# Kernel tuning notes

Measured on AMD Instinct MI355X. Metric: run time of the kernel, lower is better.

## Reference

```python
import jax, jax.numpy as jnp
import numpy as np

N, E = 50000, 800000
IN_DIM, HID, OUT, HEADS = 128, 128, 64, 4
C1 = HID // HEADS  # 32 per-head channels in gat1
NEG_SLOPE = 0.2


def _gat_conv(x, src, dst, W, a_src, a_dst, b, heads, ch):
    """PyG GATConv (inference): gather -> edge attention -> segment softmax -> scatter."""
    n = x.shape[0]
    h = (x @ W).reshape(n, heads, ch)                      # [N,H,C]
    alpha_src = jnp.einsum('nhc,hc->nh', h, a_src)         # [N,H]
    alpha_dst = jnp.einsum('nhc,hc->nh', h, a_dst)         # [N,H]
    e = jax.nn.leaky_relu(alpha_src[src] + alpha_dst[dst], NEG_SLOPE)  # [E,H]
    m = jax.ops.segment_max(e, dst, num_segments=n)        # per-target max (stable softmax)
    e = jnp.exp(e - m[dst])
    denom = jax.ops.segment_sum(e, dst, num_segments=n)
    alpha = e / (denom[dst] + 1e-16)                       # [E,H]
    out = jax.ops.segment_sum(h[src] * alpha[:, :, None], dst, num_segments=n)  # [N,H,C]
    return out.reshape(n, heads * ch) + b


def setup_inputs() -> dict:
    key = jax.random.key(0)
    ks = jax.random.split(key, 16)
    x = jax.random.normal(ks[0], (N, IN_DIM), dtype=jnp.float32)
    edge_index = jax.random.randint(ks[1], (2, E), 0, N, dtype=jnp.int64)
    s = lambda fan_in: 1.0 / np.sqrt(fan_in)
    return {
        'x': x,
        'edge_index': edge_index,
        'W1': jax.random.normal(ks[2], (IN_DIM, HEADS * C1), jnp.float32) * s(IN_DIM),
        'a_src1': jax.random.normal(ks[3], (HEADS, C1), jnp.float32) * s(C1),
        'a_dst1': jax.random.normal(ks[4], (HEADS, C1), jnp.float32) * s(C1),
        'b1': jnp.zeros((HID,), jnp.float32),
        'W2': jax.random.normal(ks[5], (HID, OUT), jnp.float32) * s(HID),
        'a_src2': jax.random.normal(ks[6], (1, OUT), jnp.float32) * s(OUT),
        'a_dst2': jax.random.normal(ks[7], (1, OUT), jnp.float32) * s(OUT),
        'b2': jnp.zeros((OUT,), jnp.float32),
        'pw1': jax.random.normal(ks[8], (OUT, OUT), jnp.float32) * s(OUT),
        'pb1': jnp.zeros((OUT,), jnp.float32),
        'pw2': jax.random.normal(ks[9], (OUT, OUT), jnp.float32) * s(OUT),
        'pb2': jnp.zeros((OUT,), jnp.float32),
    }


def reference(x, edge_index, W1, a_src1, a_dst1, b1, W2, a_src2, a_dst2, b2, pw1, pb1, pw2, pb2):
    n = x.shape[0]
    # PyG GATConv add_self_loops=True
    loops = jnp.arange(n, dtype=edge_index.dtype)
    src = jnp.concatenate([edge_index[0], loops])
    dst = jnp.concatenate([edge_index[1], loops])
    h = jax.nn.elu(_gat_conv(x, src, dst, W1, a_src1, a_dst1, b1, HEADS, C1))
    h = jax.nn.elu(_gat_conv(h, src, dst, W2, a_src2, a_dst2, b2, 1, OUT))
    # origin_proj: Linear -> ReLU -> Linear
    h = jax.nn.relu(h @ pw1 + pb1)
    return h @ pw2 + pb2
```

## Files before the change

### kernel.cpp

```cpp
#include <hip/hip_runtime.h>
#include <math.h>

#define N_NODES 50000
#define N_EDGES 800000
#define ET (N_EDGES + N_NODES)
#define IN_DIM 128
#define HID 128
#define OUT_DIM 64
#define BW 64
#define NBUCK ((N_NODES + BW - 1) / BW)
#define NBLK 256
#define EPB 3328

__device__ __forceinline__ float lrelu(float x){ return x >= 0.f ? x : 0.2f * x; }
__device__ __forceinline__ float eluf(float x){ return x > 0.f ? x : expm1f(x); }
__device__ __forceinline__ unsigned f2bf(float f){
    unsigned u = __float_as_uint(f);
    return (u + 0x7fffu + ((u >> 16) & 1u)) >> 16;
}
__device__ __forceinline__ float bflo(unsigned u){ return __uint_as_float(u << 16); }
__device__ __forceinline__ float bfhi(unsigned u){ return __uint_as_float(u & 0xffff0000u); }

__global__ __launch_bounds__(256) void k_count(const int* __restrict__ dst, int* __restrict__ C)
{
    __shared__ int cnt[NBUCK];
    const int tid = threadIdx.x, blk = blockIdx.x;
    for (int i = tid; i < NBUCK; i += 256) cnt[i] = 0;
    __syncthreads();
    #pragma unroll
    for (int j = 0; j < EPB / 256; j++) {
        const int e = blk * EPB + j * 256 + tid;
        if (e < ET) {
            const int d = (e < N_EDGES) ? dst[e] : (e - N_EDGES);
            atomicAdd(&cnt[d >> 6], 1);
        }
    }
    __syncthreads();
    for (int b = tid; b < NBUCK; b += 256) C[b * NBLK + blk] = cnt[b];
}

__global__ __launch_bounds__(256) void k_bsumA(const int* __restrict__ C, int* __restrict__ bsum2)
{
    __shared__ int red[4];
    int v = C[blockIdx.x * NBLK + threadIdx.x];
    #pragma unroll
    for (int off = 32; off > 0; off >>= 1) v += __shfl_down(v, off);
    if ((threadIdx.x & 63) == 0) red[threadIdx.x >> 6] = v;
    __syncthreads();
    if (threadIdx.x == 0) bsum2[blockIdx.x] = red[0] + red[1] + red[2] + red[3];
}

__global__ __launch_bounds__(1024) void k_bscanB(const int* __restrict__ bsum2, int* __restrict__ boff2)
{
    __shared__ int part[1024];
    const int t = threadIdx.x;
    int v = (t < NBUCK) ? bsum2[t] : 0;
    part[t] = v;
    __syncthreads();
    #pragma unroll
    for (int d = 1; d < 1024; d <<= 1) {
        int add = (t >= d) ? part[t - d] : 0;
        __syncthreads();
        part[t] += add;
        __syncthreads();
    }
    if (t < NBUCK) boff2[t] = part[t] - v;
    if (t == 0) boff2[NBUCK] = ET;
}

__global__ __launch_bounds__(256) void k_cscanC(const int* __restrict__ C,
                                                const int* __restrict__ boff2,
                                                int* __restrict__ Cs)
{
    __shared__ int part[256];
    const int t = threadIdx.x, b = blockIdx.x;
    int v = C[b * NBLK + t];
    part[t] = v;
    __syncthreads();
    #pragma unroll
    for (int d = 1; d < 256; d <<= 1) {
        int add = (t >= d) ? part[t - d] : 0;
        __syncthreads();
        part[t] += add;
        __syncthreads();
    }
    Cs[b * NBLK + t] = boff2[b] + part[t] - v;
}

__global__ __launch_bounds__(256) void k_part2(const int* __restrict__ src,
                                               const int* __restrict__ dst,
                                               const int* __restrict__ Cs,
                                               uint2* __restrict__ part)
{
    __shared__ int base[NBUCK];
    __shared__ int cnt[NBUCK];
    const int tid = threadIdx.x, blk = blockIdx.x;
    for (int b = tid; b < NBUCK; b += 256) { base[b] = Cs[b * NBLK + blk]; cnt[b] = 0; }
    __syncthreads();
    #pragma unroll
    for (int j = 0; j < EPB / 256; j++) {
        const int e = blk * EPB + j * 256 + tid;
        if (e < ET) {
            int s, d;
            if (e < N_EDGES) { s = src[e]; d = dst[e]; } else { s = d = e - N_EDGES; }
            const int b = d >> 6;
            const int r = atomicAdd(&cnt[b], 1);
            part[base[b] + r] = make_uint2((unsigned)d, (unsigned)s);
        }
    }
}

__global__ __launch_bounds__(256) void k_scat2(const int* __restrict__ boff2,
                                               const uint2* __restrict__ part,
                                               int* __restrict__ rowptr,
                                               int* __restrict__ csr_src)
{
    __shared__ int cnt64[BW];
    __shared__ int nbase[BW];
    const int b = blockIdx.x, tid = threadIdx.x;
    const int n0 = b * BW;
    const int lo = boff2[b], hi = boff2[b + 1];
    if (tid < BW) cnt64[tid] = 0;
    __syncthreads();
    for (int i = lo + tid; i < hi; i += 256) {
        atomicAdd(&cnt64[part[i].x & (BW - 1)], 1);
    }
    __syncthreads();
    if (tid < BW) {
        int v = cnt64[tid];
        int incl = v;
        #pragma unroll
        for (int off = 1; off < 64; off <<= 1) {
            int t2 = __shfl_up(incl, off);
            if (tid >= off) incl += t2;
        }
        const int excl = incl - v;
        nbase[tid] = excl;
        const int n = n0 + tid;
        if (n < N_NODES) rowptr[n] = lo + excl;
        cnt64[tid] = 0;
    }
    if (b == 0 && tid == 0) rowptr[N_NODES] = ET;
    __syncthreads();
    for (int i = lo + tid; i < hi; i += 256) {
        const uint2 p = part[i];
        const int dn = (int)p.x & (BW - 1);
        const int r = atomicAdd(&cnt64[dn], 1);
        csr_src[lo + nbase[dn] + r] = (int)p.y;
    }
}

__global__ __launch_bounds__(256, 3) void k_gemm1(
    const float* __restrict__ x, const float* __restrict__ W1,
    const float* __restrict__ a_s, const float* __restrict__ a_d,
    unsigned* __restrict__ h1b, float* __restrict__ as1, float* __restrict__ ad1)
{
    __shared__ float sW[32 * 128];
    __shared__ float sx[128 * 32];
    float4* sW4 = (float4*)sW;
    float4* sx4 = (float4*)sx;
    const float4* x4  = (const float4*)x;
    const float4* W14 = (const float4*)W1;
    const int tid = threadIdx.x;
    const int cg = tid & 15;
    const int ng = tid >> 4;
    const int axor = ng & 7;
    const int n0 = blockIdx.x * 128;

    float4 acc[8][2];
    #pragma unroll
    for (int m = 0; m < 8; m++) { acc[m][0] = make_float4(0,0,0,0); acc[m][1] = make_float4(0,0,0,0); }

    for (int c = 0; c < 4; c++) {
        __syncthreads();
        #pragma unroll
        for (int j = 0; j < 4; j++) {
            const int idx = tid + 256 * j;
            float4 v = W14[c * 1024 + idx];
            const int k = idx >> 5, f = idx & 31;
            sW4[k * 32 + ((f & 1) << 4) + (f >> 1)] = v;
        }
        #pragma unroll
        for (int j = 0; j < 4; j++) {
            const int idx = tid + 256 * j;
            const int node = idx >> 3, q = idx & 7;
            const int n = n0 + node;
            float4 v = make_float4(0,0,0,0);
            if (n < N_NODES) v = x4[n * 32 + c * 8 + q];
            sx4[node * 8 + (q ^ ((node >> 3) & 7))] = v;
        }
        __syncthreads();
        #pragma unroll 2
        for (int k4 = 0; k4 < 8; k4++) {
            float4 w0[4], w1[4];
            #pragma unroll
            for (int ks = 0; ks < 4; ks++) {
                w0[ks] = sW4[(4 * k4 + ks) * 32 + cg];
                w1[ks] = sW4[(4 * k4 + ks) * 32 + 16 + cg];
            }
            float4 xv[8];
            #pragma unroll
            for (int m = 0; m < 8; m++) xv[m] = sx4[(8 * ng + m) * 8 + (k4 ^ axor)];
            #pragma unroll
            for (int m = 0; m < 8; m++) {
                const float4 xm = xv[m];
                #define FMA8(S, KS) \
                    acc[m][0].x = fmaf(S, w0[KS].x, acc[m][0].x); \
                    acc[m][0].y = fmaf(S, w0[KS].y, acc[m][0].y); \
                    acc[m][0].z = fmaf(S, w0[KS].z, acc[m][0].z); \
                    acc[m][0].w = fmaf(S, w0[KS].w, acc[m][0].w); \
                    acc[m][1].x = fmaf(S, w1[KS].x, acc[m][1].x); \
                    acc[m][1].y = fmaf(S, w1[KS].y, acc[m][1].y); \
                    acc[m][1].z = fmaf(S, w1[KS].z, acc[m][1].z); \
                    acc[m][1].w = fmaf(S, w1[KS].w, acc[m][1].w);
                FMA8(xm.x, 0) FMA8(xm.y, 1) FMA8(xm.z, 2) FMA8(xm.w, 3)
                #undef FMA8
            }
        }
    }

    const float4 as_a = ((const float4*)a_s)[2 * cg], as_b = ((const float4*)a_s)[2 * cg + 1];
    const float4 ad_a = ((const float4*)a_d)[2 * cg], ad_b = ((const float4*)a_d)[2 * cg + 1];
    #pragma unroll
    for (int m = 0; m < 8; m++) {
        const int n = n0 + 8 * ng + m;
        float ps = acc[m][0].x * as_a.x + acc[m][0].y * as_a.y + acc[m][0].z * as_a.z + acc[m][0].w * as_a.w
                 + acc[m][1].x * as_b.x + acc[m][1].y * as_b.y + acc[m][1].z * as_b.z + acc[m][1].w * as_b.w;
        float pd = acc[m][0].x * ad_a.x + acc[m][0].y * ad_a.y + acc[m][0].z * ad_a.z + acc[m][0].w * ad_a.w
                 + acc[m][1].x * ad_b.x + acc[m][1].y * ad_b.y + acc[m][1].z * ad_b.z + acc[m][1].w * ad_b.w;
        ps += __shfl_xor(ps, 1); ps += __shfl_xor(ps, 2);
        pd += __shfl_xor(pd, 1); pd += __shfl_xor(pd, 2);
        if (n < N_NODES) {
            uint4 pk;
            pk.x = f2bf(acc[m][0].x) | (f2bf(acc[m][0].y) << 16);
            pk.y = f2bf(acc[m][0].z) | (f2bf(acc[m][0].w) << 16);
            pk.z = f2bf(acc[m][1].x) | (f2bf(acc[m][1].y) << 16);
            pk.w = f2bf(acc[m][1].z) | (f2bf(acc[m][1].w) << 16);
            ((uint4*)h1b)[n * 16 + cg] = pk;
            if ((cg & 3) == 0) {
                as1[n * 4 + (cg >> 2)] = ps;
                ad1[n * 4 + (cg >> 2)] = pd;
            }
        }
    }
}

__global__ __launch_bounds__(256) void k_aggr1(
    const int* __restrict__ rowptr, const int* __restrict__ csr_src,
    const float* __restrict__ as1, const float* __restrict__ ad1,
    const uint4* __restrict__ h1u4, float* __restrict__ acc1)
{
    const int d  = blockIdx.x * 16 + (threadIdx.x >> 4);
    const int c8 = threadIdx.x & 15;
    const int hd = c8 >> 2;
    const int r0 = rowptr[d], r1 = rowptr[d + 1];
    const float adv = ad1[d * 4 + hd];
    float den = 0.f;
    float acc[8];
    #pragma unroll
    for (int m = 0; m < 8; m++) acc[m] = 0.f;
    int i = r0;
    for (; i + 2 <= r1; i += 2) {
        const int s0 = csr_src[i], s1 = csr_src[i + 1];
        const float e0 = as1[s0 * 4 + hd], e1 = as1[s1 * 4 + hd];
        const uint4 u0 = h1u4[s0 * 16 + c8];
        const uint4 u1 = h1u4[s1 * 16 + c8];
        const float w0 = expf(lrelu(e0 + adv));
        const float w1 = expf(lrelu(e1 + adv));
        den += w0 + w1;
        acc[0] = fmaf(bflo(u0.x), w0, acc[0]); acc[1] = fmaf(bfhi(u0.x), w0, acc[1]);
        acc[2] = fmaf(bflo(u0.y), w0, acc[2]); acc[3] = fmaf(bfhi(u0.y), w0, acc[3]);
        acc[4] = fmaf(bflo(u0.z), w0, acc[4]); acc[5] = fmaf(bfhi(u0.z), w0, acc[5]);
        acc[6] = fmaf(bflo(u0.w), w0, acc[6]); acc[7] = fmaf(bfhi(u0.w), w0, acc[7]);
        acc[0] = fmaf(bflo(u1.x), w1, acc[0]); acc[1] = fmaf(bfhi(u1.x), w1, acc[1]);
        acc[2] = fmaf(bflo(u1.y), w1, acc[2]); acc[3] = fmaf(bfhi(u1.y), w1, acc[3]);
        acc[4] = fmaf(bflo(u1.z), w1, acc[4]); acc[5] = fmaf(bfhi(u1.z), w1, acc[5]);
        acc[6] = fmaf(bflo(u1.w), w1, acc[6]); acc[7] = fmaf(bfhi(u1.w), w1, acc[7]);
    }
    if (i < r1) {
        const int s = csr_src[i];
        const float w = expf(lrelu(as1[s * 4 + hd] + adv));
        const uint4 u = h1u4[s * 16 + c8];
        den += w;
        acc[0] = fmaf(bflo(u.x), w, acc[0]); acc[1] = fmaf(bfhi(u.x), w, acc[1]);
        acc[2] = fmaf(bflo(u.y), w, acc[2]); acc[3] = fmaf(bfhi(u.y), w, acc[3]);
        acc[4] = fmaf(bflo(u.z), w, acc[4]); acc[5] = fmaf(bfhi(u.z), w, acc[5]);
        acc[6] = fmaf(bflo(u.w), w, acc[6]); acc[7] = fmaf(bfhi(u.w), w, acc[7]);
    }
    const float inv = 1.f / (den + 1e-16f);
    float4 o0 = make_float4(acc[0] * inv, acc[1] * inv, acc[2] * inv, acc[3] * inv);
    float4 o1 = make_float4(acc[4] * inv, acc[5] * inv, acc[6] * inv, acc[7] * inv);
    ((float4*)acc1)[d * 32 + 2 * c8 + 0] = o0;
    ((float4*)acc1)[d * 32 + 2 * c8 + 1] = o1;
}

__global__ __launch_bounds__(256, 4) void k_layer2(
    const float* __restrict__ acc1, const float* __restrict__ b1,
    const float* __restrict__ W2, const float* __restrict__ a_s2, const float* __restrict__ a_d2,
    unsigned* __restrict__ h2b, float* __restrict__ as2, float* __restrict__ ad2)
{
    __shared__ float sW[32 * 64];
    __shared__ float sx[128 * 32];
    float4* sW4 = (float4*)sW;
    float4* sx4 = (float4*)sx;
    const float4* a14 = (const float4*)acc1;
    const float4* W24 = (const float4*)W2;
    const float4* b14 = (const float4*)b1;
    const int tid = threadIdx.x;
    const int cg = tid & 7;
    const int ng = tid >> 3;
    const int n0 = blockIdx.x * 128;

    float4 acc[4][2];
    #pragma unroll
    for (int m = 0; m < 4; m++) { acc[m][0] = make_float4(0,0,0,0); acc[m][1] = make_float4(0,0,0,0); }

    for (int c = 0; c < 4; c++) {
        __syncthreads();
        #pragma unroll
        for (int j = 0; j < 2; j++) {
            const int idx = tid + 256 * j;
            float4 v = W24[c * 512 + idx];
            const int k = idx >> 4, f = idx & 15;
            sW4[k * 16 + ((f & 1) << 3) + (f >> 1)] = v;
        }
        #pragma unroll
        for (int j = 0; j < 4; j++) {
            const int idx = tid + 256 * j;
            const int node = idx >> 3, q = idx & 7;
            const int n = n0 + node;
            float4 v = make_float4(0,0,0,0);
            if (n < N_NODES) {
                v = a14[n * 32 + c * 8 + q];
                const float4 bb = b14[c * 8 + q];
                v.x = eluf(v.x + bb.x);
                v.y = eluf(v.y + bb.y);
                v.z = eluf(v.z + bb.z);
                v.w = eluf(v.w + bb.w);
            }
            sx4[node * 8 + (q ^ ((node >> 3) & 7))] = v;
        }
        __syncthreads();
        #pragma unroll 2
        for (int k4 = 0; k4 < 8; k4++) {
            float4 w0[4], w1[4];
            #pragma unroll
            for (int ks = 0; ks < 4; ks++) {
                w0[ks] = sW4[(4 * k4 + ks) * 16 + cg];
                w1[ks] = sW4[(4 * k4 + ks) * 16 + 8 + cg];
            }
            float4 xv[4];
            #pragma unroll
            for (int m = 0; m < 4; m++) {
                const int node = 4 * ng + m;
                xv[m] = sx4[node * 8 + (k4 ^ ((node >> 3) & 7))];
            }
            #pragma unroll
            for (int m = 0; m < 4; m++) {
                const float4 xm = xv[m];
                #define FMA8(S, KS) \
                    acc[m][0].x = fmaf(S, w0[KS].x, acc[m][0].x); \
                    acc[m][0].y = fmaf(S, w0[KS].y, acc[m][0].y); \
                    acc[m][0].z = fmaf(S, w0[KS].z, acc[m][0].z); \
                    acc[m][0].w = fmaf(S, w0[KS].w, acc[m][0].w); \
                    acc[m][1].x = fmaf(S, w1[KS].x, acc[m][1].x); \
                    acc[m][1].y = fmaf(S, w1[KS].y, acc[m][1].y); \
                    acc[m][1].z = fmaf(S, w1[KS].z, acc[m][1].z); \
                    acc[m][1].w = fmaf(S, w1[KS].w, acc[m][1].w);
                FMA8(xm.x, 0) FMA8(xm.y, 1) FMA8(xm.z, 2) FMA8(xm.w, 3)
                #undef FMA8
            }
        }
    }

    const float4 as_a = ((const float4*)a_s2)[2 * cg], as_b = ((const float4*)a_s2)[2 * cg + 1];
    const float4 ad_a = ((const float4*)a_d2)[2 * cg], ad_b = ((const float4*)a_d2)[2 * cg + 1];
    #pragma unroll
    for (int m = 0; m < 4; m++) {
        const int n = n0 + 4 * ng + m;
        float ps = acc[m][0].x * as_a.x + acc[m][0].y * as_a.y + acc[m][0].z * as_a.z + acc[m][0].w * as_a.w
                 + acc[m][1].x * as_b.x + acc[m][1].y * as_b.y + acc[m][1].z * as_b.z + acc[m][1].w * as_b.w;
        float pd = acc[m][0].x * ad_a.x + acc[m][0].y * ad_a.y + acc[m][0].z * ad_a.z + acc[m][0].w * ad_a.w
                 + acc[m][1].x * ad_b.x + acc[m][1].y * ad_b.y + acc[m][1].z * ad_b.z + acc[m][1].w * ad_b.w;
        ps += __shfl_xor(ps, 1); ps += __shfl_xor(ps, 2); ps += __shfl_xor(ps, 4);
        pd += __shfl_xor(pd, 1); pd += __shfl_xor(pd, 2); pd += __shfl_xor(pd, 4);
        if (n < N_NODES) {
            uint4 pk;
            pk.x = f2bf(acc[m][0].x) | (f2bf(acc[m][0].y) << 16);
            pk.y = f2bf(acc[m][0].z) | (f2bf(acc[m][0].w) << 16);
            pk.z = f2bf(acc[m][1].x) | (f2bf(acc[m][1].y) << 16);
            pk.w = f2bf(acc[m][1].z) | (f2bf(acc[m][1].w) << 16);
            ((uint4*)h2b)[n * 8 + cg] = pk;
            if (cg == 0) { as2[n] = ps; ad2[n] = pd; }
        }
    }
}

__global__ __launch_bounds__(256) void k_aggr2(
    const int* __restrict__ rowptr, const int* __restrict__ csr_src,
    const float* __restrict__ as2, const float* __restrict__ ad2,
    const uint4* __restrict__ h2u4, float* __restrict__ acc2)
{
    const int d  = blockIdx.x * 32 + (threadIdx.x >> 3);
    const int c8 = threadIdx.x & 7;
    if (d >= N_NODES) return;
    const int r0 = rowptr[d], r1 = rowptr[d + 1];
    const float adv = ad2[d];
    float den = 0.f;
    float acc[8];
    #pragma unroll
    for (int m = 0; m < 8; m++) acc[m] = 0.f;
    int i = r0;
    for (; i + 2 <= r1; i += 2) {
        const int s0 = csr_src[i], s1 = csr_src[i + 1];
        const float e0 = as2[s0], e1 = as2[s1];
        const uint4 u0 = h2u4[s0 * 8 + c8];
        const uint4 u1 = h2u4[s1 * 8 + c8];
        const float w0 = expf(lrelu(e0 + adv));
        const float w1 = expf(lrelu(e1 + adv));
        den += w0 + w1;
        acc[0] = fmaf(bflo(u0.x), w0, acc[0]); acc[1] = fmaf(bfhi(u0.x), w0, acc[1]);
        acc[2] = fmaf(bflo(u0.y), w0, acc[2]); acc[3] = fmaf(bfhi(u0.y), w0, acc[3]);
        acc[4] = fmaf(bflo(u0.z), w0, acc[4]); acc[5] = fmaf(bfhi(u0.z), w0, acc[5]);
        acc[6] = fmaf(bflo(u0.w), w0, acc[6]); acc[7] = fmaf(bfhi(u0.w), w0, acc[7]);
        acc[0] = fmaf(bflo(u1.x), w1, acc[0]); acc[1] = fmaf(bfhi(u1.x), w1, acc[1]);
        acc[2] = fmaf(bflo(u1.y), w1, acc[2]); acc[3] = fmaf(bfhi(u1.y), w1, acc[3]);
        acc[4] = fmaf(bflo(u1.z), w1, acc[4]); acc[5] = fmaf(bfhi(u1.z), w1, acc[5]);
        acc[6] = fmaf(bflo(u1.w), w1, acc[6]); acc[7] = fmaf(bfhi(u1.w), w1, acc[7]);
    }
    if (i < r1) {
        const int s = csr_src[i];
        const float w = expf(lrelu(as2[s] + adv));
        const uint4 u = h2u4[s * 8 + c8];
        den += w;
        acc[0] = fmaf(bflo(u.x), w, acc[0]); acc[1] = fmaf(bfhi(u.x), w, acc[1]);
        acc[2] = fmaf(bflo(u.y), w, acc[2]); acc[3] = fmaf(bfhi(u.y), w, acc[3]);
        acc[4] = fmaf(bflo(u.z), w, acc[4]); acc[5] = fmaf(bfhi(u.z), w, acc[5]);
        acc[6] = fmaf(bflo(u.w), w, acc[6]); acc[7] = fmaf(bfhi(u.w), w, acc[7]);
    }
    const float inv = 1.f / (den + 1e-16f);
    float4 o0 = make_float4(acc[0] * inv, acc[1] * inv, acc[2] * inv, acc[3] * inv);
    float4 o1 = make_float4(acc[4] * inv, acc[5] * inv, acc[6] * inv, acc[7] * inv);
    ((float4*)acc2)[d * 16 + 2 * c8 + 0] = o0;
    ((float4*)acc2)[d * 16 + 2 * c8 + 1] = o1;
}

__global__ __launch_bounds__(256, 2) void k_out(
    const float* __restrict__ acc2, const float* __restrict__ b2,
    const float* __restrict__ pw1, const float* __restrict__ pb1,
    const float* __restrict__ pw2, const float* __restrict__ pb2,
    float* __restrict__ out)
{
    __shared__ float s1[64 * 64];
    __shared__ float s2[64 * 64];
    __shared__ float so[64][68];
    __shared__ float sp[64][68];
    const int tid = threadIdx.x;
    for (int i = tid; i < 1024; i += 256) {
        ((float4*)s1)[i] = ((const float4*)pw1)[i];
        ((float4*)s2)[i] = ((const float4*)pw2)[i];
    }
    const int cg = tid & 15;
    const int ng = tid >> 4;
    const float4 pb1_4 = ((const float4*)pb1)[cg];
    const float4 pb2_4 = ((const float4*)pb2)[cg];
    const int nGroups = (N_NODES + 63) / 64;
    for (int g = blockIdx.x; g < nGroups; g += gridDim.x) {
        const int n0 = g * 64;
        __syncthreads();
        #pragma unroll
        for (int j = 0; j < 4; j++) {
            const int i = tid + 256 * j;
            const int node = i >> 4, quad = i & 15;
            const int n = n0 + node;
            float4 v = make_float4(0.f, 0.f, 0.f, 0.f);
            if (n < N_NODES) {
                v = ((const float4*)acc2)[n * 16 + quad];
                const float4 bb = ((const float4*)b2)[quad];
                v.x = eluf(v.x + bb.x);
                v.y = eluf(v.y + bb.y);
                v.z = eluf(v.z + bb.z);
                v.w = eluf(v.w + bb.w);
            }
            *(float4*)&so[node][4 * quad] = v;
        }
        __syncthreads();
        float4 p[4];
        #pragma unroll
        for (int m = 0; m < 4; m++) p[m] = pb1_4;
        #pragma unroll 8
        for (int k = 0; k < 64; k++) {
            const float4 w = *(const float4*)&s1[k * 64 + 4 * cg];
            #pragma unroll
            for (int m = 0; m < 4; m++) {
                const float xv = so[4 * ng + m][k];
                p[m].x = fmaf(xv, w.x, p[m].x);
                p[m].y = fmaf(xv, w.y, p[m].y);
                p[m].z = fmaf(xv, w.z, p[m].z);
                p[m].w = fmaf(xv, w.w, p[m].w);
            }
        }
        #pragma unroll
        for (int m = 0; m < 4; m++) {
            p[m].x = fmaxf(p[m].x, 0.f); p[m].y = fmaxf(p[m].y, 0.f);
            p[m].z = fmaxf(p[m].z, 0.f); p[m].w = fmaxf(p[m].w, 0.f);
            *(float4*)&sp[4 * ng + m][4 * cg] = p[m];
        }
        __syncthreads();
        float4 o[4];
        #pragma unroll
        for (int m = 0; m < 4; m++) o[m] = pb2_4;
        #pragma unroll 8
        for (int k = 0; k < 64; k++) {
            const float4 w = *(const float4*)&s2[k * 64 + 4 * cg];
            #pragma unroll
            for (int m = 0; m < 4; m++) {
                const float xv = sp[4 * ng + m][k];
                o[m].x = fmaf(xv, w.x, o[m].x);
                o[m].y = fmaf(xv, w.y, o[m].y);
                o[m].z = fmaf(xv, w.z, o[m].z);
                o[m].w = fmaf(xv, w.w, o[m].w);
            }
        }
        #pragma unroll
        for (int m = 0; m < 4; m++) {
            const int n = n0 + 4 * ng + m;
            if (n < N_NODES) ((float4*)out)[n * 16 + cg] = o[m];
        }
    }
}

extern "C" void kernel_launch(void* const* d_in, const int* in_sizes, int n_in,
                              void* d_out, int out_size, void* d_ws, size_t ws_size,
                              hipStream_t stream)
{
    const float* x      = (const float*)d_in[0];
    const int*   ei     = (const int*)d_in[1];
    const int*   src    = ei;
    const int*   dst    = ei + N_EDGES;
    const float* W1     = (const float*)d_in[2];
    const float* a_src1 = (const float*)d_in[3];
    const float* a_dst1 = (const float*)d_in[4];
    const float* b1     = (const float*)d_in[5];
    const float* W2     = (const float*)d_in[6];
    const float* a_src2 = (const float*)d_in[7];
    const float* a_dst2 = (const float*)d_in[8];
    const float* b2     = (const float*)d_in[9];
    const float* pw1    = (const float*)d_in[10];
    const float* pb1    = (const float*)d_in[11];
    const float* pw2    = (const float*)d_in[12];
    const float* pb2    = (const float*)d_in[13];

    uint2* part  = (uint2*)d_ws;
    int* ibase   = (int*)(part + ET);
    int* rowptr  = ibase;
    int* C       = rowptr + 50001;
    int* Cs      = C + 200192;
    int* bsum2   = Cs + 200192;
    int* boff2   = bsum2 + 782;
    int* csr_src = boff2 + 785;
    unsigned* h1b = (unsigned*)(csr_src + 850000);
    unsigned* h2b = h1b + 3200000;
    float* fws   = (float*)(h2b + 1600000);
    float* as1   = fws;
    float* ad1   = as1 + 200000;
    float* acc1  = ad1 + 200000;
    float* as2   = acc1 + 6400000;
    float* ad2   = as2 + 50000;
    float* acc2  = ad2 + 50000;

    k_count<<<NBLK, 256, 0, stream>>>(dst, C);
    k_bsumA<<<NBUCK, 256, 0, stream>>>(C, bsum2);
    k_bscanB<<<1, 1024, 0, stream>>>(bsum2, boff2);
    k_cscanC<<<NBUCK, 256, 0, stream>>>(C, boff2, Cs);
    k_part2<<<NBLK, 256, 0, stream>>>(src, dst, Cs, part);
    k_scat2<<<NBUCK, 256, 0, stream>>>(boff2, part, rowptr, csr_src);

    k_gemm1<<<(N_NODES + 127) / 128, 256, 0, stream>>>(x, W1, a_src1, a_dst1, h1b, as1, ad1);
    k_aggr1<<<N_NODES / 16, 256, 0, stream>>>(rowptr, csr_src, as1, ad1,
                                              (const uint4*)h1b, acc1);

    k_layer2<<<(N_NODES + 127) / 128, 256, 0, stream>>>(acc1, b1, W2, a_src2, a_dst2, h2b, as2, ad2);
    k_aggr2<<<(N_NODES + 31) / 32, 256, 0, stream>>>(rowptr, csr_src, as2, ad2,
                                                     (const uint4*)h2b, acc2);

    k_out<<<782, 256, 0, stream>>>(acc2, b2, pw1, pb1, pw2, pb2, (float*)d_out);
}
```

Measured before the change: 265.8 us.

## Rewrite layer-1 GEMM with bf16 MFMA 16x16x32 instructions

Replaces the FP32 FMA register-tiled GEMM in k_gemm1 with bf16 MFMA matrix-core instructions. x and W1 are converted to bf16 and staged in padded shared memory, and each wave computes a 16x128 output tile. The attention logits are then reduced across lanes with shuffles. This trades FP32 input precision for matrix-core throughput, restages the whole W1 in every block, and writes h1 as scattered 16-bit stores instead of 128-bit vectors. The layer-2 packing change is cosmetic.

```diff
diff --git a/kernel.cpp b/kernel.cpp
--- a/kernel.cpp
+++ b/kernel.cpp
@@ -12,6 +12,9 @@
 #define NBLK 256
 #define EPB 3328
 
+typedef __attribute__((ext_vector_type(8))) short bf16x8;
+typedef __attribute__((ext_vector_type(4))) float f32x4;
+
 __device__ __forceinline__ float lrelu(float x){ return x >= 0.f ? x : 0.2f * x; }
 __device__ __forceinline__ float eluf(float x){ return x > 0.f ? x : expm1f(x); }
 __device__ __forceinline__ unsigned f2bf(float f){
@@ -150,96 +153,85 @@
     }
 }
 
-__global__ __launch_bounds__(256, 3) void k_gemm1(
+__global__ __launch_bounds__(256, 2) void k_gemm1(
     const float* __restrict__ x, const float* __restrict__ W1,
     const float* __restrict__ a_s, const float* __restrict__ a_d,
     unsigned* __restrict__ h1b, float* __restrict__ as1, float* __restrict__ ad1)
 {
-    __shared__ float sW[32 * 128];
-    __shared__ float sx[128 * 32];
-    float4* sW4 = (float4*)sW;
-    float4* sx4 = (float4*)sx;
-    const float4* x4  = (const float4*)x;
-    const float4* W14 = (const float4*)W1;
+    __shared__ unsigned sWt[128 * 68];
+    __shared__ unsigned sxb[64 * 68];
     const int tid = threadIdx.x;
-    const int cg = tid & 15;
-    const int ng = tid >> 4;
-    const int axor = ng & 7;
-    const int n0 = blockIdx.x * 128;
-
-    float4 acc[8][2];
-    #pragma unroll
-    for (int m = 0; m < 8; m++) { acc[m][0] = make_float4(0,0,0,0); acc[m][1] = make_float4(0,0,0,0); }
-
-    for (int c = 0; c < 4; c++) {
-        __syncthreads();
-        #pragma unroll
-        for (int j = 0; j < 4; j++) {
-            const int idx = tid + 256 * j;
-            float4 v = W14[c * 1024 + idx];
-            const int k = idx >> 5, f = idx & 31;
-            sW4[k * 32 + ((f & 1) << 4) + (f >> 1)] = v;
-        }
-        #pragma unroll
-        for (int j = 0; j < 4; j++) {
-            const int idx = tid + 256 * j;
-            const int node = idx >> 3, q = idx & 7;
-            const int n = n0 + node;
-            float4 v = make_float4(0,0,0,0);
-            if (n < N_NODES) v = x4[n * 32 + c * 8 + q];
-            sx4[node * 8 + (q ^ ((node >> 3) & 7))] = v;
-        }
-        __syncthreads();
-        #pragma unroll 2
-        for (int k4 = 0; k4 < 8; k4++) {
-            float4 w0[4], w1[4];
+    const int wave = tid >> 6;
+    const int lane = tid & 63;
+    const int ll   = lane & 15;
+    const int quad = lane >> 4;
+    const int n0 = blockIdx.x * 64;
+
+    for (int idx = tid; idx < 8192; idx += 256) {
+        const int n = idx & 127, kp = idx >> 7;
+        const float w0 = W1[(2 * kp) * 128 + n];
+        const float w1 = W1[(2 * kp + 1) * 128 + n];
+        sWt[n * 68 + kp] = f2bf(w0) | (f2bf(w1) << 16);
+    }
+    for (int idx = tid; idx < 4096; idx += 256) {
+        const int node = idx >> 6, kp = idx & 63;
+        const int n = n0 + node;
+        unsigned pk = 0;
+        if (n < N_NODES) {
+            const float x0 = x[n * 128 + 2 * kp];
+            const float x1 = x[n * 128 + 2 * kp + 1];
+            pk = f2bf(x0) | (f2bf(x1) << 16);
+        }
+        sxb[node * 68 + kp] = pk;
+    }
+    __syncthreads();
+
+    f32x4 acc[8];
+    #pragma unroll
+    for (int t = 0; t < 8; t++) acc[t] = (f32x4){0.f, 0.f, 0.f, 0.f};
+
+    #pragma unroll
+    for (int kk = 0; kk < 4; kk++) {
+        const int kpo = 16 * kk + 4 * quad;
+        const bf16x8 a = *(const bf16x8*)&sxb[(16 * wave + ll) * 68 + kpo];
+        #pragma unroll
+        for (int t = 0; t < 8; t++) {
+            const bf16x8 b = *(const bf16x8*)&sWt[(16 * t + ll) * 68 + kpo];
+            acc[t] = __builtin_amdgcn_mfma_f32_16x16x32_bf16(a, b, acc[t], 0, 0, 0);
+        }
+    }
+
+    float as_v[8], ad_v[8];
+    #pragma unroll
+    for (int t = 0; t < 8; t++) { as_v[t] = a_s[16 * t + ll]; ad_v[t] = a_d[16 * t + ll]; }
+    unsigned short* h1u = (unsigned short*)h1b;
+    #pragma unroll
+    for (int r = 0; r < 4; r++) {
+        const int n = n0 + 16 * wave + 4 * quad + r;
+        float ps0 = acc[0][r] * as_v[0] + acc[1][r] * as_v[1];
+        float ps1 = acc[2][r] * as_v[2] + acc[3][r] * as_v[3];
+        float ps2 = acc[4][r] * as_v[4] + acc[5][r] * as_v[5];
+        float ps3 = acc[6][r] * as_v[6] + acc[7][r] * as_v[7];
+        float pd0 = acc[0][r] * ad_v[0] + acc[1][r] * ad_v[1];
+        float pd1 = acc[2][r] * ad_v[2] + acc[3][r] * ad_v[3];
+        float pd2 = acc[4][r] * ad_v[4] + acc[5][r] * ad_v[5];
+        float pd3 = acc[6][r] * ad_v[6] + acc[7][r] * ad_v[7];
+        #pragma unroll
+        for (int off = 1; off < 16; off <<= 1) {
+            ps0 += __shfl_xor(ps0, off); ps1 += __shfl_xor(ps1, off);
+            ps2 += __shfl_xor(ps2, off); ps3 += __shfl_xor(ps3, off);
+            pd0 += __shfl_xor(pd0, off); pd1 += __shfl_xor(pd1, off);
+            pd2 += __shfl_xor(pd2, off); pd3 += __shfl_xor(pd3, off);
+        }
+        if (n < N_NODES) {
             #pragma unroll
-            for (int ks = 0; ks < 4; ks++) {
-                w0[ks] = sW4[(4 * k4 + ks) * 32 + cg];
-                w1[ks] = sW4[(4 * k4 + ks) * 32 + 16 + cg];
-            }
-            float4 xv[8];
-            #pragma unroll
-            for (int m = 0; m < 8; m++) xv[m] = sx4[(8 * ng + m) * 8 + (k4 ^ axor)];
-            #pragma unroll
-            for (int m = 0; m < 8; m++) {
-                const float4 xm = xv[m];
-                #define FMA8(S, KS) \
-                    acc[m][0].x = fmaf(S, w0[KS].x, acc[m][0].x); \
-                    acc[m][0].y = fmaf(S, w0[KS].y, acc[m][0].y); \
-                    acc[m][0].z = fmaf(S, w0[KS].z, acc[m][0].z); \
-                    acc[m][0].w = fmaf(S, w0[KS].w, acc[m][0].w); \
-                    acc[m][1].x = fmaf(S, w1[KS].x, acc[m][1].x); \
-                    acc[m][1].y = fmaf(S, w1[KS].y, acc[m][1].y); \
-                    acc[m][1].z = fmaf(S, w1[KS].z, acc[m][1].z); \
-                    acc[m][1].w = fmaf(S, w1[KS].w, acc[m][1].w);
-                FMA8(xm.x, 0) FMA8(xm.y, 1) FMA8(xm.z, 2) FMA8(xm.w, 3)
-                #undef FMA8
-            }
-        }
-    }
-
-    const float4 as_a = ((const float4*)a_s)[2 * cg], as_b = ((const float4*)a_s)[2 * cg + 1];
-    const float4 ad_a = ((const float4*)a_d)[2 * cg], ad_b = ((const float4*)a_d)[2 * cg + 1];
-    #pragma unroll
-    for (int m = 0; m < 8; m++) {
-        const int n = n0 + 8 * ng + m;
-        float ps = acc[m][0].x * as_a.x + acc[m][0].y * as_a.y + acc[m][0].z * as_a.z + acc[m][0].w * as_a.w
-                 + acc[m][1].x * as_b.x + acc[m][1].y * as_b.y + acc[m][1].z * as_b.z + acc[m][1].w * as_b.w;
-        float pd = acc[m][0].x * ad_a.x + acc[m][0].y * ad_a.y + acc[m][0].z * ad_a.z + acc[m][0].w * ad_a.w
-                 + acc[m][1].x * ad_b.x + acc[m][1].y * ad_b.y + acc[m][1].z * ad_b.z + acc[m][1].w * ad_b.w;
-        ps += __shfl_xor(ps, 1); ps += __shfl_xor(ps, 2);
-        pd += __shfl_xor(pd, 1); pd += __shfl_xor(pd, 2);
-        if (n < N_NODES) {
-            uint4 pk;
-            pk.x = f2bf(acc[m][0].x) | (f2bf(acc[m][0].y) << 16);
-            pk.y = f2bf(acc[m][0].z) | (f2bf(acc[m][0].w) << 16);
-            pk.z = f2bf(acc[m][1].x) | (f2bf(acc[m][1].y) << 16);
-            pk.w = f2bf(acc[m][1].z) | (f2bf(acc[m][1].w) << 16);
-            ((uint4*)h1b)[n * 16 + cg] = pk;
-            if ((cg & 3) == 0) {
-                as1[n * 4 + (cg >> 2)] = ps;
-                ad1[n * 4 + (cg >> 2)] = pd;
+            for (int t = 0; t < 8; t++)
+                h1u[n * 128 + 16 * t + ll] = (unsigned short)f2bf(acc[t][r]);
+            if (ll == 0) {
+                as1[n * 4 + 0] = ps0; as1[n * 4 + 1] = ps1;
+                as1[n * 4 + 2] = ps2; as1[n * 4 + 3] = ps3;
+                ad1[n * 4 + 0] = pd0; ad1[n * 4 + 1] = pd1;
+                ad1[n * 4 + 2] = pd2; ad1[n * 4 + 3] = pd3;
             }
         }
     }
@@ -385,12 +377,14 @@
         ps += __shfl_xor(ps, 1); ps += __shfl_xor(ps, 2); ps += __shfl_xor(ps, 4);
         pd += __shfl_xor(pd, 1); pd += __shfl_xor(pd, 2); pd += __shfl_xor(pd, 4);
         if (n < N_NODES) {
-            uint4 pk;
+            uint2 pk;
             pk.x = f2bf(acc[m][0].x) | (f2bf(acc[m][0].y) << 16);
             pk.y = f2bf(acc[m][0].z) | (f2bf(acc[m][0].w) << 16);
-            pk.z = f2bf(acc[m][1].x) | (f2bf(acc[m][1].y) << 16);
-            pk.w = f2bf(acc[m][1].z) | (f2bf(acc[m][1].w) << 16);
-            ((uint4*)h2b)[n * 8 + cg] = pk;
+            uint2 pk2;
+            pk2.x = f2bf(acc[m][1].x) | (f2bf(acc[m][1].y) << 16);
+            pk2.y = f2bf(acc[m][1].z) | (f2bf(acc[m][1].w) << 16);
+            uint4 pk4 = make_uint4(pk.x, pk.y, pk2.x, pk2.y);
+            ((uint4*)h2b)[n * 8 + cg] = pk4;
             if (cg == 0) { as2[n] = ps; ad2[n] = pd; }
         }
     }
@@ -576,7 +570,7 @@
     k_part2<<<NBLK, 256, 0, stream>>>(src, dst, Cs, part);
     k_scat2<<<NBUCK, 256, 0, stream>>>(boff2, part, rowptr, csr_src);
 
-    k_gemm1<<<(N_NODES + 127) / 128, 256, 0, stream>>>(x, W1, a_src1, a_dst1, h1b, as1, ad1);
+    k_gemm1<<<(N_NODES + 63) / 64, 256, 0, stream>>>(x, W1, a_src1, a_dst1, h1b, as1, ad1);
     k_aggr1<<<N_NODES / 16, 256, 0, stream>>>(rowptr, csr_src, as1, ad1,
                                               (const uint4*)h1b, acc1);
 
```

New measurement: 258.6 us. 1.03x faster.
